# Optimization experiments

Measured on AMD Instinct MI355X. Metric: run time of the kernel, lower is better.

## Reference

```python
import jax, jax.numpy as jnp
import numpy as np

SCALES = [3, 5, 7, 9]


def _conv1d(x, w, b, k):
    # x: (BN, 1, L), w: (1, 1, k), b: (1,) -> (BN, 1, L), 'same' padding (k//2)
    y = jax.lax.conv_general_dilated(
        x, w, window_strides=(1,), padding=[(k // 2, k // 2)],
        dimension_numbers=("NCH", "OIH", "NCH"))
    return y + b[None, :, None]


def setup_inputs() -> dict:
    key = jax.random.key(0)
    ks = jax.random.split(key, 16)
    B, N, L = 64, 321, 720
    inp = {"x": jax.random.normal(ks[0], (B, N, L), dtype=jnp.float32)}
    # Conv1d(1,1,k) params, kaiming-ish scale 1/sqrt(k)
    for i, s in enumerate(SCALES):
        inp[f"cw{i}"] = jax.random.normal(ks[1 + 2 * i], (1, 1, s), dtype=jnp.float32) / np.sqrt(s)
        inp[f"cb{i}"] = jax.random.normal(ks[2 + 2 * i], (1,), dtype=jnp.float32) * 0.01
    # weight_net: Linear(4,32) -> ReLU -> Linear(32,4) -> Softmax
    inp["W1"] = jax.random.normal(ks[10], (4, 32), dtype=jnp.float32) / np.sqrt(4.0)
    inp["b1"] = jnp.zeros((32,), dtype=jnp.float32)
    inp["W2"] = jax.random.normal(ks[11], (32, 4), dtype=jnp.float32) / np.sqrt(32.0)
    inp["b2"] = jnp.zeros((4,), dtype=jnp.float32)
    return inp


def reference(x, cw0, cb0, cw1, cb1, cw2, cb2, cw3, cb3, W1, b1, W2, b2):
    B, N, L = x.shape
    xf = x.reshape(B * N, 1, L)
    cparams = [(cw0, cb0), (cw1, cb1), (cw2, cb2), (cw3, cb3)]
    feats, ents = [], []
    for (w, b), k in zip(cparams, SCALES):
        f = _conv1d(xf, w, b, k)                      # (BN, 1, L)
        prob = jax.nn.softmax(f, axis=-1)
        ent = -(prob * jnp.log(prob + 1e-8)).sum(axis=-1)  # (BN, 1)
        feats.append(f)
        ents.append(ent)
    entropy_vec = jnp.concatenate(ents, axis=-1)      # (BN, 4)
    h = jax.nn.relu(entropy_vec @ W1 + b1)
    weights = jax.nn.softmax(h @ W2 + b2, axis=-1)    # (BN, 4)
    stacked = jnp.stack(feats, axis=1)                # (BN, 4, 1, L)
    trend = (stacked * weights[:, :, None, None]).sum(axis=1)  # (BN, 1, L)
    return trend.reshape(B, N, L)
```

## Files before the change

kernel.cpp:

```cpp
#include <hip/hip_runtime.h>
#include <math.h>

#define NT 64
#define L_LEN 720
#define NROWS (64 * 321)

#define LOG2E 1.4426950408889634f
#define LN2   0.6931471805599453f

typedef float f32x2 __attribute__((ext_vector_type(2)));

__device__ __forceinline__ f32x2 pkfma(f32x2 a, f32x2 b, f32x2 c) {
    return __builtin_elementwise_fma(a, b, c);
}

template<int CTRL, int RM>
__device__ __forceinline__ float dpp_add(float x) {
    int t = __builtin_amdgcn_update_dpp(0, __float_as_int(x), CTRL, RM, 0xf, true);
    return x + __int_as_float(t);
}

__device__ __forceinline__ float wave_sum64(float x) {
    x = dpp_add<0x111, 0xf>(x);
    x = dpp_add<0x112, 0xf>(x);
    x = dpp_add<0x114, 0xf>(x);
    x = dpp_add<0x118, 0xf>(x);
    x = dpp_add<0x142, 0xa>(x);
    x = dpp_add<0x143, 0xc>(x);
    return __int_as_float(__builtin_amdgcn_readlane(__float_as_int(x), 63));
}

__device__ __forceinline__ float half_sum32(float x) {
    x = dpp_add<0x111, 0xf>(x);
    x = dpp_add<0x112, 0xf>(x);
    x = dpp_add<0x114, 0xf>(x);
    x = dpp_add<0x118, 0xf>(x);
    x = dpp_add<0x142, 0xa>(x);
    return __int_as_float(__builtin_amdgcn_readlane(__float_as_int(x), 31));
}

__global__ __launch_bounds__(NT, 4) void trend_kernel(
    const float* __restrict__ x,
    const float* __restrict__ cw0, const float* __restrict__ cb0,
    const float* __restrict__ cw1, const float* __restrict__ cb1,
    const float* __restrict__ cw2, const float* __restrict__ cb2,
    const float* __restrict__ cw3, const float* __restrict__ cb3,
    const float* __restrict__ W1, const float* __restrict__ b1,
    const float* __restrict__ W2, const float* __restrict__ b2,
    float* __restrict__ out)
{
    const int lane = threadIdx.x;
    const int row  = blockIdx.x;

    const float* __restrict__ xr = x + (size_t)row * L_LEN;

    const int ll = (lane < 60) ? lane : 59;
    const int e0 = 12 * ll - 4;
    float xw[20];
#pragma unroll
    for (int q = 0; q < 5; ++q) {
        int e = e0 + 4 * q;
        e = (e < 0) ? 0 : ((e > L_LEN - 4) ? (L_LEN - 4) : e);
        float4 v = *(const float4*)(xr + e);
        xw[4 * q + 0] = v.x; xw[4 * q + 1] = v.y;
        xw[4 * q + 2] = v.z; xw[4 * q + 3] = v.w;
    }

    const float* cws[4] = {cw0, cw1, cw2, cw3};
    const float* cbs[4] = {cb0, cb1, cb2, cb3};
    float w2[4][9], bs2[4];
#pragma unroll
    for (int s = 0; s < 4; ++s) {
        const int k = 3 + 2 * s;
        bs2[s] = cbs[s][0] * LOG2E;
#pragma unroll
        for (int t = 0; t < 9; ++t)
            w2[s][t] = (t < k) ? (cws[s][t] * LOG2E) : 0.0f;
    }

    if (lane == 0)  { xw[0] = 0.f; xw[1] = 0.f; xw[2] = 0.f; xw[3] = 0.f; }
    if (lane == 59) { xw[16] = 0.f; xw[17] = 0.f; xw[18] = 0.f; xw[19] = 0.f; }

#pragma unroll
    for (int t = 0; t < 20; ++t) asm volatile("" : "+v"(xw[t]));

    f32x2 xp[10], xo[9];
#pragma unroll
    for (int i = 0; i < 10; ++i) xp[i] = (f32x2){xw[2 * i], xw[2 * i + 1]};
#pragma unroll
    for (int i = 0; i < 9; ++i)  xo[i] = (f32x2){xw[2 * i + 1], xw[2 * i + 2]};

    f32x2 Spk[4]  = {{0.f,0.f},{0.f,0.f},{0.f,0.f},{0.f,0.f}};
    f32x2 Tpk[4]  = {{0.f,0.f},{0.f,0.f},{0.f,0.f},{0.f,0.f}};
#pragma unroll
    for (int j = 0; j < 6; ++j) {
#pragma unroll
        for (int s = 0; s < 4; ++s) {
            const int k = 3 + 2 * s;
            const int off = 3 - s;
            f32x2 u = (f32x2){bs2[s], bs2[s]};
#pragma unroll
            for (int t = 0; t < k; ++t) {
                const int st = 2 * j + off + t;
                const f32x2 p = (st & 1) ? xo[st >> 1] : xp[st >> 1];
                const f32x2 wv = (f32x2){w2[s][t], w2[s][t]};
                u = pkfma(wv, p, u);
            }
            f32x2 ev;
            ev.x = __builtin_amdgcn_exp2f(u.x);
            ev.y = __builtin_amdgcn_exp2f(u.y);
            Spk[s] += ev;
            Tpk[s] = pkfma(u, ev, Tpk[s]);
        }
    }

    const bool active = lane < 60;
    float S[4], Tu[4];
#pragma unroll
    for (int s = 0; s < 4; ++s) {
        S[s]  = active ? (Spk[s].x + Spk[s].y) : 0.0f;
        Tu[s] = active ? (Tpk[s].x + Tpk[s].y) : 0.0f;
    }

    float ent[4];
#pragma unroll
    for (int s = 0; s < 4; ++s) {
        float Sg = wave_sum64(S[s]);
        float Tg = wave_sum64(Tu[s]);
        ent[s] = LN2 * (__builtin_amdgcn_logf(Sg)
                        - Tg * __builtin_amdgcn_rcpf(Sg));
    }

    const int hidx = lane & 31;
    float h = b1[hidx];
#pragma unroll
    for (int s = 0; s < 4; ++s) h = fmaf(ent[s], W1[s * 32 + hidx], h);
    h = fmaxf(h, 0.0f);

    const float4 w2v = ((const float4*)W2)[hidx];
    float lg0 = half_sum32(h * w2v.x) + b2[0];
    float lg1 = half_sum32(h * w2v.y) + b2[1];
    float lg2 = half_sum32(h * w2v.z) + b2[2];
    float lg3 = half_sum32(h * w2v.w) + b2[3];

    float m = fmaxf(fmaxf(lg0, lg1), fmaxf(lg2, lg3));
    float e0w = __expf(lg0 - m), e1w = __expf(lg1 - m);
    float e2w = __expf(lg2 - m), e3w = __expf(lg3 - m);
    float inv = LN2 / (e0w + e1w + e2w + e3w);
    const float wgt[4] = {e0w * inv, e1w * inv, e2w * inv, e3w * inv};

    float Wm[9] = {0,0,0,0,0,0,0,0,0};
    float Bm = 0.f;
#pragma unroll
    for (int s = 0; s < 4; ++s) {
        const int k = 3 + 2 * s;
        const int off = 3 - s;
#pragma unroll
        for (int t = 0; t < k; ++t)
            Wm[off + t] = fmaf(wgt[s], w2[s][t], Wm[off + t]);
        Bm = fmaf(wgt[s], bs2[s], Bm);
    }

    if (active) {
        float* __restrict__ orow = out + (size_t)row * L_LEN + 12 * lane;
        f32x2 o[6];
#pragma unroll
        for (int j = 0; j < 6; ++j) {
            f32x2 acc = (f32x2){Bm, Bm};
#pragma unroll
            for (int d = 0; d < 9; ++d) {
                const int st = 2 * j + d;
                const f32x2 p = (st & 1) ? xo[st >> 1] : xp[st >> 1];
                const f32x2 wv = (f32x2){Wm[d], Wm[d]};
                acc = pkfma(wv, p, acc);
            }
            o[j] = acc;
        }
#pragma unroll
        for (int q = 0; q < 3; ++q) {
            float4 v;
            v.x = o[2 * q].x;     v.y = o[2 * q].y;
            v.z = o[2 * q + 1].x; v.w = o[2 * q + 1].y;
            *(float4*)(orow + 4 * q) = v;
        }
    }
}

extern "C" void kernel_launch(void* const* d_in, const int* in_sizes, int n_in,
                              void* d_out, int out_size, void* d_ws, size_t ws_size,
                              hipStream_t stream) {
    const float* xp  = (const float*)d_in[0];
    const float* cw0 = (const float*)d_in[1];
    const float* cb0 = (const float*)d_in[2];
    const float* cw1 = (const float*)d_in[3];
    const float* cb1 = (const float*)d_in[4];
    const float* cw2 = (const float*)d_in[5];
    const float* cb2 = (const float*)d_in[6];
    const float* cw3 = (const float*)d_in[7];
    const float* cb3 = (const float*)d_in[8];
    const float* W1  = (const float*)d_in[9];
    const float* b1  = (const float*)d_in[10];
    const float* W2  = (const float*)d_in[11];
    const float* b2  = (const float*)d_in[12];
    float* outp = (float*)d_out;

    trend_kernel<<<NROWS, NT, 0, stream>>>(xp, cw0, cb0, cw1, cb1, cw2, cb2,
                                           cw3, cb3, W1, b1, W2, b2, outp);
}
```

Measured before the change: 33.60 us.

## Reuse per-scale conv outputs for final mix and repack packed-FMA operand pairs

Keeps each scale's conv outputs in registers and builds the final trend as a 4-term weighted sum of them, instead of recomputing a fused 9-tap convolution with mixed weights. Packed operands now pair elements i and i+6, so every tap reads one pre-built register pair and the separate even/odd register arrays go away. Conv weights are forced to scalar registers with readfirstlane. This cuts post-softmax FMAs and operand shuffling, but holds 24 more packed values live across the wave reductions, which raises VGPR pressure and may affect occupancy.

New measurement: 32.90 us, median of 2. -2.1%, faster.

```diff
diff --git a/kernel.cpp b/kernel.cpp
--- a/kernel.cpp
+++ b/kernel.cpp
@@ -12,6 +12,10 @@
 
 __device__ __forceinline__ f32x2 pkfma(f32x2 a, f32x2 b, f32x2 c) {
     return __builtin_elementwise_fma(a, b, c);
+}
+
+__device__ __forceinline__ float rfl(float v) {
+    return __int_as_float(__builtin_amdgcn_readfirstlane(__float_as_int(v)));
 }
 
 template<int CTRL, int RM>
@@ -72,10 +76,10 @@
 #pragma unroll
     for (int s = 0; s < 4; ++s) {
         const int k = 3 + 2 * s;
-        bs2[s] = cbs[s][0] * LOG2E;
+        bs2[s] = rfl(cbs[s][0] * LOG2E);
 #pragma unroll
         for (int t = 0; t < 9; ++t)
-            w2[s][t] = (t < k) ? (cws[s][t] * LOG2E) : 0.0f;
+            w2[s][t] = (t < k) ? rfl(cws[s][t] * LOG2E) : 0.0f;
     }
 
     if (lane == 0)  { xw[0] = 0.f; xw[1] = 0.f; xw[2] = 0.f; xw[3] = 0.f; }
@@ -84,14 +88,13 @@
 #pragma unroll
     for (int t = 0; t < 20; ++t) asm volatile("" : "+v"(xw[t]));
 
-    f32x2 xp[10], xo[9];
-#pragma unroll
-    for (int i = 0; i < 10; ++i) xp[i] = (f32x2){xw[2 * i], xw[2 * i + 1]};
-#pragma unroll
-    for (int i = 0; i < 9; ++i)  xo[i] = (f32x2){xw[2 * i + 1], xw[2 * i + 2]};
-
-    f32x2 Spk[4]  = {{0.f,0.f},{0.f,0.f},{0.f,0.f},{0.f,0.f}};
-    f32x2 Tpk[4]  = {{0.f,0.f},{0.f,0.f},{0.f,0.f},{0.f,0.f}};
+    f32x2 p[14];
+#pragma unroll
+    for (int i = 0; i < 14; ++i) p[i] = (f32x2){xw[i], xw[i + 6]};
+
+    f32x2 fu[4][6];
+    f32x2 Spk[4] = {{0.f,0.f},{0.f,0.f},{0.f,0.f},{0.f,0.f}};
+    f32x2 Tpk[4] = {{0.f,0.f},{0.f,0.f},{0.f,0.f},{0.f,0.f}};
 #pragma unroll
     for (int j = 0; j < 6; ++j) {
 #pragma unroll
@@ -101,11 +104,10 @@
             f32x2 u = (f32x2){bs2[s], bs2[s]};
 #pragma unroll
             for (int t = 0; t < k; ++t) {
-                const int st = 2 * j + off + t;
-                const f32x2 p = (st & 1) ? xo[st >> 1] : xp[st >> 1];
                 const f32x2 wv = (f32x2){w2[s][t], w2[s][t]};
-                u = pkfma(wv, p, u);
+                u = pkfma(wv, p[j + off + t], u);
             }
+            fu[s][j] = u;
             f32x2 ev;
             ev.x = __builtin_amdgcn_exp2f(u.x);
             ev.y = __builtin_amdgcn_exp2f(u.y);
@@ -114,6 +116,14 @@
         }
     }
 
+#pragma unroll
+    for (int s = 0; s < 4; ++s)
+#pragma unroll
+        for (int j = 0; j < 6; ++j) {
+            asm volatile("" : "+v"(fu[s][j].x));
+            asm volatile("" : "+v"(fu[s][j].y));
+        }
+
     const bool active = lane < 60;
     float S[4], Tu[4];
 #pragma unroll
@@ -147,42 +157,26 @@
     float e0w = __expf(lg0 - m), e1w = __expf(lg1 - m);
     float e2w = __expf(lg2 - m), e3w = __expf(lg3 - m);
     float inv = LN2 / (e0w + e1w + e2w + e3w);
-    const float wgt[4] = {e0w * inv, e1w * inv, e2w * inv, e3w * inv};
-
-    float Wm[9] = {0,0,0,0,0,0,0,0,0};
-    float Bm = 0.f;
-#pragma unroll
-    for (int s = 0; s < 4; ++s) {
-        const int k = 3 + 2 * s;
-        const int off = 3 - s;
-#pragma unroll
-        for (int t = 0; t < k; ++t)
-            Wm[off + t] = fmaf(wgt[s], w2[s][t], Wm[off + t]);
-        Bm = fmaf(wgt[s], bs2[s], Bm);
-    }
+    const float wg0 = e0w * inv, wg1 = e1w * inv;
+    const float wg2 = e2w * inv, wg3 = e3w * inv;
 
     if (active) {
-        float* __restrict__ orow = out + (size_t)row * L_LEN + 12 * lane;
         f32x2 o[6];
 #pragma unroll
         for (int j = 0; j < 6; ++j) {
-            f32x2 acc = (f32x2){Bm, Bm};
-#pragma unroll
-            for (int d = 0; d < 9; ++d) {
-                const int st = 2 * j + d;
-                const f32x2 p = (st & 1) ? xo[st >> 1] : xp[st >> 1];
-                const f32x2 wv = (f32x2){Wm[d], Wm[d]};
-                acc = pkfma(wv, p, acc);
-            }
+            f32x2 acc = (f32x2){wg0, wg0} * fu[0][j];
+            acc = pkfma((f32x2){wg1, wg1}, fu[1][j], acc);
+            acc = pkfma((f32x2){wg2, wg2}, fu[2][j], acc);
+            acc = pkfma((f32x2){wg3, wg3}, fu[3][j], acc);
             o[j] = acc;
         }
-#pragma unroll
-        for (int q = 0; q < 3; ++q) {
-            float4 v;
-            v.x = o[2 * q].x;     v.y = o[2 * q].y;
-            v.z = o[2 * q + 1].x; v.w = o[2 * q + 1].y;
-            *(float4*)(orow + 4 * q) = v;
-        }
+        float* __restrict__ orow = out + (size_t)row * L_LEN + 12 * lane;
+        float4 v0 = {o[0].x, o[1].x, o[2].x, o[3].x};
+        float4 v1 = {o[4].x, o[5].x, o[0].y, o[1].y};
+        float4 v2 = {o[2].y, o[3].y, o[4].y, o[5].y};
+        *(float4*)(orow)     = v0;
+        *(float4*)(orow + 4) = v1;
+        *(float4*)(orow + 8) = v2;
     }
 }
 
```
